# Kernel tuning notes

Measured on AMD Instinct MI355X. Metric: run time of the kernel, lower is better.

The kernel has to match this reference:

```python
import jax, jax.numpy as jnp
import numpy as np

B, S, V, E, H = 128, 128, 8000, 512, 2048
GIVEN = 64


def setup_inputs() -> dict:
    key = jax.random.key(0)
    ks = jax.random.split(key, 13)
    def p(i, shape):
        return (jax.random.normal(ks[i], shape, jnp.float32) * 0.02)
    return {
        "x": jax.random.randint(ks[0], (B, S), 0, V, jnp.int32),
        "class_label": jax.random.randint(ks[1], (B,), 0, 2, jnp.int32),
        "given_num": GIVEN,
        "emb": p(2, (V, E)),
        "Wih0": p(3, (4 * H, E)), "Whh0": p(4, (4 * H, H)),
        "bih0": p(5, (4 * H,)), "bhh0": p(6, (4 * H,)),
        "Wih1": p(7, (4 * H, H)), "Whh1": p(8, (4 * H, H)),
        "bih1": p(9, (4 * H,)), "bhh1": p(10, (4 * H,)),
        "Wlin": p(11, (V, H)), "blin": p(12, (V,)),
    }


def _cell(xt, h, c, Wih, Whh, bih, bhh):
    # PyTorch LSTMCell math, gate order (i, f, g, o)
    g = xt @ Wih.T + h @ Whh.T + (bih + bhh)
    i, f, gg, o = jnp.split(g, 4, axis=-1)
    c = jax.nn.sigmoid(f) * c + jax.nn.sigmoid(i) * jnp.tanh(gg)
    h = jax.nn.sigmoid(o) * jnp.tanh(c)
    return h, c


def reference(x, class_label, given_num, emb, Wih0, Whh0, bih0, bhh0,
              Wih1, Whh1, bih1, bhh1, Wlin, blin):
    Bb, Ss = x.shape
    Hh = Whh0.shape[1]
    z = jnp.zeros((Bb, Hh), dtype=emb.dtype)
    init = (z, z, z, z)  # (h0, c0, h1, c1) for 2-layer LSTM

    def two_layer(carry, te):
        h0, c0, h1, c1 = carry
        h0, c0 = _cell(te, h0, c0, Wih0, Whh0, bih0, bhh0)
        h1, c1 = _cell(h0, h1, c1, Wih1, Whh1, bih1, bhh1)
        return (h0, c0, h1, c1)

    # Teacher-forced prefix: feed ground-truth tokens for i < given_num
    seq_e = emb[x[:, :given_num]]  # (B, given_num, E)
    def tf_step(carry, te):
        return two_layer(carry, te), None
    carry, _ = jax.lax.scan(tf_step, init, seq_e.swapaxes(0, 1))

    # Rollout: sample from softmax(logits) each step (multinomial == categorical)
    te0 = emb[x[:, given_num - 1]]  # (B, E)
    keys = jax.random.split(jax.random.key(1), Ss - given_num)

    def roll_step(carry, k):
        (h0, c0, h1, c1), te = carry
        h0, c0, h1, c1 = two_layer((h0, c0, h1, c1), te)
        logits = h1 @ Wlin.T + blin  # (B, V)
        nt = jax.random.categorical(k, logits)  # (B,)
        return ((h0, c0, h1, c1), emb[nt]), nt

    _, toks = jax.lax.scan(roll_step, (carry, te0), keys)  # (S-given, B)
    return jnp.concatenate([x[:, :given_num], toks.T.astype(x.dtype)], axis=1)
```

## Files before the change

### kernel.cpp

```cpp
#include <hip/hip_runtime.h>
#include <stdint.h>
#include <math.h>

#define B_     128
#define S_     128
#define V_     8000
#define E_     512
#define H_     2048
#define H4_    8192
#define GIVEN_ 64

typedef __bf16 bf16x8 __attribute__((ext_vector_type(8)));
typedef float  f32x16 __attribute__((ext_vector_type(16)));
typedef short  short8 __attribute__((ext_vector_type(8)));

__device__ __forceinline__ uint32_t rotl32(uint32_t v, int d) {
  return (v << d) | (v >> (32 - d));
}

__device__ __forceinline__ void threefry2x32(uint32_t k0, uint32_t k1,
                                             uint32_t x0, uint32_t x1,
                                             uint32_t& o0, uint32_t& o1) {
  uint32_t k2 = k0 ^ k1 ^ 0x1BD11BDAu;
  x0 += k0; x1 += k1;
#define TF_RND(R) { x0 += x1; x1 = rotl32(x1, (R)); x1 ^= x0; }
  TF_RND(13) TF_RND(15) TF_RND(26) TF_RND(6)
  x0 += k1; x1 += k2 + 1u;
  TF_RND(17) TF_RND(29) TF_RND(16) TF_RND(24)
  x0 += k2; x1 += k0 + 2u;
  TF_RND(13) TF_RND(15) TF_RND(26) TF_RND(6)
  x0 += k0; x1 += k1 + 3u;
  TF_RND(17) TF_RND(29) TF_RND(16) TF_RND(24)
  x0 += k1; x1 += k2 + 4u;
  TF_RND(13) TF_RND(15) TF_RND(26) TF_RND(6)
  x0 += k2; x1 += k0 + 5u;
#undef TF_RND
  o0 = x0; o1 = x1;
}

__global__ void keys_kernel(uint32_t* __restrict__ keys) {
  int t = threadIdx.x;
  uint32_t o0, o1;
  threefry2x32(0u, 1u, 0u, (uint32_t)t, o0, o1);
  keys[2 * t]     = o0;
  keys[2 * t + 1] = o1;
}

__global__ void copy_prefix(const int* __restrict__ x, int* __restrict__ out) {
  int idx = blockIdx.x * blockDim.x + threadIdx.x;
  int b = idx >> 6;
  int s = idx & 63;
  out[b * S_ + s] = x[b * S_ + s];
}

__device__ __forceinline__ void split2(float x, uint16_t& hi, uint16_t& lo) {
  uint32_t xb = __float_as_uint(x);
  hi = (uint16_t)(xb >> 16);
  float l = x - __uint_as_float(xb & 0xFFFF0000u);
  lo = (uint16_t)(__float_as_uint(l) >> 16);
}

__device__ __forceinline__ void splitpack(float4 a, float4 b,
                                          bf16x8& hi, bf16x8& lo) {
  float e[8] = {a.x, a.y, a.z, a.w, b.x, b.y, b.z, b.w};
  short8 h, l;
#pragma unroll
  for (int j = 0; j < 8; ++j) {
    uint16_t h16, l16;
    split2(e[j], h16, l16);
    h[j] = (short)h16;
    l[j] = (short)l16;
  }
  hi = __builtin_bit_cast(bf16x8, h);
  lo = __builtin_bit_cast(bf16x8, l);
}

__device__ __forceinline__ void unpack3(short8 hv, uint2 m, bf16x8& bh, bf16x8& bl) {
  short8 lv;
#pragma unroll
  for (int j = 0; j < 8; ++j) {
    uint32_t hbits = ((uint32_t)(uint16_t)hv[j]) << 16;
    uint32_t mbyte = ((j < 4 ? (m.x >> (8 * j)) : (m.y >> (8 * (j - 4)))) & 0xFFu);
    float xf = __uint_as_float(hbits | (mbyte << 8));
    float lf = xf - __uint_as_float(hbits);
    lv[j] = (short)(__float_as_uint(lf) >> 16);
  }
  bh = __builtin_bit_cast(bf16x8, hv);
  bl = __builtin_bit_cast(bf16x8, lv);
}

__global__ void pack3_panel(
    const float* __restrict__ W, uint16_t* __restrict__ PH,
    uint8_t* __restrict__ PM, int K, int nks, int gateRe)
{
  const int bid = blockIdx.x;
  const int jb = bid / nks, ks = bid - jb * nks;
  const int t = threadIdx.x;
  const int lrow = t & 31, lgrp = t >> 5;
  const int wrow = gateRe ? ((lrow >> 3) * H_ + jb * 8 + (lrow & 7))
                          : (jb * 32 + lrow);
  const float* src = W + (size_t)wrow * K + ks * 16 + lgrp * 8;
  float4 a = ((const float4*)src)[0];
  float4 b = ((const float4*)src)[1];
  float e[8] = {a.x, a.y, a.z, a.w, b.x, b.y, b.z, b.w};
  short8 h;
  uint32_t mlo = 0, mhi = 0;
#pragma unroll
  for (int j = 0; j < 8; ++j) {
    uint32_t xb = __float_as_uint(e[j]);
    h[j] = (short)(xb >> 16);
    uint32_t mb = (xb >> 8) & 0xFFu;
    if (j < 4) mlo |= mb << (8 * j);
    else       mhi |= mb << (8 * (j - 4));
  }
  const size_t bi = ((size_t)bid * 64 + t) * 8;
  *(short8*)&PH[bi] = h;
  *(uint2*)&PM[bi] = make_uint2(mlo, mhi);
}

#define MFMA_(a, b, c) __builtin_amdgcn_mfma_f32_32x32x16_bf16(a, b, c, 0, 0, 0)

template<bool GATHER>
__device__ __forceinline__ void run_phase_p(
    f32x16 (&acc)[4],
    const float* __restrict__ aF,
    const uint16_t* __restrict__ aHi, const uint16_t* __restrict__ aLo,
    const int* __restrict__ ridx, int rstride,
    const uint16_t* __restrict__ PH, const uint8_t* __restrict__ PM,
    int K, int jb, int w, int lane, int lrow, int lgrp)
{
  const int nFS = K >> 7;
  const size_t bbase = (size_t)jb * (K >> 4);

  size_t aoff0, aoff1, aoff2, aoff3;
  if (GATHER) {
    aoff0 = (size_t)ridx[(size_t)(lrow)      * rstride] * E_ + lgrp * 8;
    aoff1 = (size_t)ridx[(size_t)(32 + lrow) * rstride] * E_ + lgrp * 8;
    aoff2 = (size_t)ridx[(size_t)(64 + lrow) * rstride] * E_ + lgrp * 8;
    aoff3 = (size_t)ridx[(size_t)(96 + lrow) * rstride] * E_ + lgrp * 8;
  } else {
    aoff0 = (size_t)lgrp * 256 + (size_t)lrow * 8;
    aoff1 = aoff0 + 512;
    aoff2 = aoff0 + 1024;
    aoff3 = aoff0 + 1536;
  }

  short8 bH[4]; uint2 bM[4];
  float4 gR0[2][2], gR1[2][2], gR2[2][2], gR3[2][2];
  bf16x8 sh0[2], sh1[2], sh2[2], sh3[2], sl0[2], sl1[2], sl2[2], sl3[2];

#define BLOAD(BUF, KS)                                                       \
  {                                                                          \
    const size_t bi = ((bbase + (size_t)(KS)) * 64 + (size_t)lane) * 8;      \
    bH[BUF] = *(const short8*)(PH + bi);                                     \
    bM[BUF] = *(const uint2*)(PM + bi);                                      \
  }

#define ALOAD(BUF, KS)                                                       \
  {                                                                          \
    if (GATHER) {                                                            \
      const float* a0 = aF + aoff0 + (size_t)(KS) * 16;                      \
      const float* a1 = aF + aoff1 + (size_t)(KS) * 16;                      \
      const float* a2 = aF + aoff2 + (size_t)(KS) * 16;                      \
      const float* a3 = aF + aoff3 + (size_t)(KS) * 16;                      \
      gR0[BUF][0] = ((const float4*)a0)[0]; gR0[BUF][1] = ((const float4*)a0)[1]; \
      gR1[BUF][0] = ((const float4*)a1)[0]; gR1[BUF][1] = ((const float4*)a1)[1]; \
      gR2[BUF][0] = ((const float4*)a2)[0]; gR2[BUF][1] = ((const float4*)a2)[1]; \
      gR3[BUF][0] = ((const float4*)a3)[0]; gR3[BUF][1] = ((const float4*)a3)[1]; \
    } else {                                                                 \
      size_t o0 = aoff0 + (size_t)(KS) * 2048;                               \
      size_t o1 = aoff1 + (size_t)(KS) * 2048;                               \
      size_t o2 = aoff2 + (size_t)(KS) * 2048;                               \
      size_t o3 = aoff3 + (size_t)(KS) * 2048;                               \
      sh0[BUF] = *(const bf16x8*)(aHi + o0); sl0[BUF] = *(const bf16x8*)(aLo + o0); \
      sh1[BUF] = *(const bf16x8*)(aHi + o1); sl1[BUF] = *(const bf16x8*)(aLo + o1); \
      sh2[BUF] = *(const bf16x8*)(aHi + o2); sl2[BUF] = *(const bf16x8*)(aLo + o2); \
      sh3[BUF] = *(const bf16x8*)(aHi + o3); sl3[BUF] = *(const bf16x8*)(aLo + o3); \
    }                                                                        \
  }

#define COMP(BB, AB)                                                         \
  {                                                                          \
    bf16x8 bh, bl;                                                           \
    unpack3(bH[BB], bM[BB], bh, bl);                                         \
    bf16x8 ah, al;                                                           \
    if (GATHER) splitpack(gR0[AB][0], gR0[AB][1], ah, al);                   \
    else { ah = sh0[AB]; al = sl0[AB]; }                                     \
    acc[0] = MFMA_(ah, bh, acc[0]);                                          \
    acc[0] = MFMA_(ah, bl, acc[0]);                                          \
    acc[0] = MFMA_(al, bh, acc[0]);                                          \
    if (GATHER) splitpack(gR1[AB][0], gR1[AB][1], ah, al);                   \
    else { ah = sh1[AB]; al = sl1[AB]; }                                     \
    acc[1] = MFMA_(ah, bh, acc[1]);                                          \
    acc[1] = MFMA_(ah, bl, acc[1]);                                          \
    acc[1] = MFMA_(al, bh, acc[1]);                                          \
    if (GATHER) splitpack(gR2[AB][0], gR2[AB][1], ah, al);                   \
    else { ah = sh2[AB]; al = sl2[AB]; }                                     \
    acc[2] = MFMA_(ah, bh, acc[2]);                                          \
    acc[2] = MFMA_(ah, bl, acc[2]);                                          \
    acc[2] = MFMA_(al, bh, acc[2]);                                          \
    if (GATHER) splitpack(gR3[AB][0], gR3[AB][1], ah, al);                   \
    else { ah = sh3[AB]; al = sl3[AB]; }                                     \
    acc[3] = MFMA_(ah, bh, acc[3]);                                          \
    acc[3] = MFMA_(ah, bl, acc[3]);                                          \
    acc[3] = MFMA_(al, bh, acc[3]);                                          \
  }

  BLOAD(0, w); BLOAD(1, w + 8); BLOAD(2, w + 16); BLOAD(3, w + 24);
  ALOAD(0, w); ALOAD(1, w + 8);
  for (int it = 0; it < nFS; it += 4) {
    const int kb = w + it * 8;
    COMP(0, 0);
    if (it + 4 < nFS) BLOAD(0, kb + 32);
    if (it + 2 < nFS) ALOAD(0, kb + 16);
    COMP(1, 1);
    if (it + 5 < nFS) BLOAD(1, kb + 40);
    if (it + 3 < nFS) ALOAD(1, kb + 24);
    COMP(2, 0);
    if (it + 6 < nFS) BLOAD(2, kb + 48);
    if (it + 4 < nFS) ALOAD(0, kb + 32);
    COMP(3, 1);
    if (it + 7 < nFS) BLOAD(3, kb + 56);
    if (it + 5 < nFS) ALOAD(1, kb + 40);
  }
#undef BLOAD
#undef ALOAD
#undef COMP
}

template<int EPI, int GATHER1>
__global__ __launch_bounds__(512, 2) void gemm_ks_p(
    const float* __restrict__ a1F,
    const uint16_t* __restrict__ a1Hi, const uint16_t* __restrict__ a1Lo,
    const int* __restrict__ ridx, int rstride,
    const uint16_t* __restrict__ PH1, const uint8_t* __restrict__ PM1, int K1,
    const uint16_t* __restrict__ a2Hi, const uint16_t* __restrict__ a2Lo,
    const uint16_t* __restrict__ PH2, const uint8_t* __restrict__ PM2, int K2,
    const float* __restrict__ bih, const float* __restrict__ bhh,
    float* __restrict__ cState,
    uint16_t* __restrict__ hOutHi, uint16_t* __restrict__ hOutLo,
    const float* __restrict__ bias, float* __restrict__ Cout)
{
  __shared__ float red[4][128 * 32];

  const int jb   = blockIdx.x;
  const int tid  = threadIdx.x;
  const int w    = tid >> 6;
  const int lane = tid & 63;
  const int lrow = lane & 31;
  const int lgrp = lane >> 5;

  f32x16 acc[4];
#pragma unroll
  for (int mf = 0; mf < 4; ++mf)
#pragma unroll
    for (int r = 0; r < 16; ++r) acc[mf][r] = 0.0f;

  run_phase_p<GATHER1 != 0>(acc, a1F, a1Hi, a1Lo, ridx, rstride,
                            PH1, PM1, K1, jb, w, lane, lrow, lgrp);
  if (K2 > 0)
    run_phase_p<false>(acc, nullptr, a2Hi, a2Lo, nullptr, 0,
                       PH2, PM2, K2, jb, w, lane, lrow, lgrp);

  const int wl = w & 3;
  if (w < 4) {
#pragma unroll
    for (int mf = 0; mf < 4; ++mf)
#pragma unroll
      for (int r = 0; r < 16; ++r) {
        const int row = mf * 32 + (r & 3) + 8 * (r >> 2) + 4 * lgrp;
        red[wl][row * 32 + (lrow ^ (row & 31))] = acc[mf][r];
      }
  }
  __syncthreads();
  if (w >= 4) {
#pragma unroll
    for (int mf = 0; mf < 4; ++mf)
#pragma unroll
      for (int r = 0; r < 16; ++r) {
        const int row = mf * 32 + (r & 3) + 8 * (r >> 2) + 4 * lgrp;
        red[wl][row * 32 + (lrow ^ (row & 31))] += acc[mf][r];
      }
  }
  __syncthreads();

  if constexpr (EPI == 1) {
    const int b  = tid & 127;
    const int uh = (tid >> 7) * 2;
#pragma unroll
    for (int q = 0; q < 2; ++q) {
      const int u = uh + q;
      float gs[4];
#pragma unroll
      for (int g = 0; g < 4; ++g) {
        const int cs = (g * 8 + u) ^ (b & 31);
        gs[g] = ((red[0][b * 32 + cs] + red[1][b * 32 + cs])
                 + red[2][b * 32 + cs]) + red[3][b * 32 + cs];
      }
      const int n = jb * 8 + u;
      float gi = gs[0] + bih[n]          + bhh[n];
      float gf = gs[1] + bih[H_ + n]     + bhh[H_ + n];
      float gg = gs[2] + bih[2 * H_ + n] + bhh[2 * H_ + n];
      float go = gs[3] + bih[3 * H_ + n] + bhh[3 * H_ + n];
      float si = 1.f / (1.f + expf(-gi));
      float sf = 1.f / (1.f + expf(-gf));
      float so = 1.f / (1.f + expf(-go));
      const size_t ci = (size_t)b * H_ + n;
      float cv = sf * cState[ci] + si * tanhf(gg);
      cState[ci] = cv;
      float hv = so * tanhf(cv);
      uint16_t hh, hl;
      split2(hv, hh, hl);
      const size_t hoff = (size_t)((n >> 4) * 4 + (b >> 5)) * 512
                        + (size_t)((n >> 3) & 1) * 256
                        + (size_t)(b & 31) * 8 + (size_t)(n & 7);
      hOutHi[hoff] = hh;
      hOutLo[hoff] = hl;
    }
  } else {
    const int b  = tid & 127;
    const int ch = (tid >> 7) * 8;
#pragma unroll
    for (int q = 0; q < 8; ++q) {
      const int col = ch + q;
      const int cs  = col ^ (b & 31);
      float v = ((red[0][b * 32 + cs] + red[1][b * 32 + cs])
                 + red[2][b * 32 + cs]) + red[3][b * 32 + cs];
      Cout[(size_t)b * V_ + jb * 32 + col] = v + bias[jb * 32 + col];
    }
  }
}

__global__ __launch_bounds__(256) void sample_kernel(
    const float* __restrict__ logits, const uint32_t* __restrict__ keys,
    int t, int* __restrict__ out, int col)
{
  const int b = blockIdx.x;
  const int tid = threadIdx.x;
  const uint32_t k0 = keys[2 * t];
  const uint32_t k1 = keys[2 * t + 1];
  const float* lrow = logits + (size_t)b * V_;

  float best = -3.4e38f;
  int bestIdx = 0;
  for (int v = tid; v < V_; v += 256) {
    uint32_t j = (uint32_t)(b * V_ + v);
    uint32_t o0, o1;
    threefry2x32(k0, k1, 0u, j, o0, o1);
    uint32_t bits = o0 ^ o1;
    float f = __uint_as_float((bits >> 9) | 0x3f800000u) - 1.0f;
    float u = fmaxf(1.17549435e-38f, f + 1.17549435e-38f);
    float t1 = (float)log((double)u);
    float t2 = -t1;
    float t3 = (float)log((double)t2);
    float val = (-t3) + lrow[v];
    if (val > best) { best = val; bestIdx = v; }
  }

  __shared__ float sv[256];
  __shared__ int   si[256];
  sv[tid] = best; si[tid] = bestIdx;
  __syncthreads();
  for (int s = 128; s > 0; s >>= 1) {
    if (tid < s) {
      float v2 = sv[tid + s]; int i2 = si[tid + s];
      if (v2 > sv[tid] || (v2 == sv[tid] && i2 < si[tid])) { sv[tid] = v2; si[tid] = i2; }
    }
    __syncthreads();
  }
  if (tid == 0) out[b * S_ + col] = si[0];
}

extern "C" void kernel_launch(void* const* d_in, const int* in_sizes, int n_in,
                              void* d_out, int out_size, void* d_ws, size_t ws_size,
                              hipStream_t stream) {
  const int*   x    = (const int*)  d_in[0];
  const float* emb  = (const float*)d_in[3];
  const float* Wih0 = (const float*)d_in[4];
  const float* Whh0 = (const float*)d_in[5];
  const float* bih0 = (const float*)d_in[6];
  const float* bhh0 = (const float*)d_in[7];
  const float* Wih1 = (const float*)d_in[8];
  const float* Whh1 = (const float*)d_in[9];
  const float* bih1 = (const float*)d_in[10];
  const float* bhh1 = (const float*)d_in[11];
  const float* Wlin = (const float*)d_in[12];
  const float* blin = (const float*)d_in[13];
  int* out = (int*)d_out;

  char* wp = (char*)d_ws;
  size_t o = 0;
  auto alloc = [&](size_t bytes) {
    void* p = wp + o; o += (bytes + 255) & ~(size_t)255; return p;
  };
  uint32_t* keys   = (uint32_t*)alloc(512);
  float*    logits = (float*)   alloc((size_t)B_ * V_ * 4);
  float*    c0     = (float*)   alloc((size_t)B_ * H_ * 4);
  float*    c1     = (float*)   alloc((size_t)B_ * H_ * 4);
  uint16_t* hS0hi[2]; uint16_t* hS0lo[2]; uint16_t* hS1hi[2]; uint16_t* hS1lo[2];
  for (int i = 0; i < 2; ++i) hS0hi[i] = (uint16_t*)alloc((size_t)B_ * H_ * 2);
  for (int i = 0; i < 2; ++i) hS0lo[i] = (uint16_t*)alloc((size_t)B_ * H_ * 2);
  for (int i = 0; i < 2; ++i) hS1hi[i] = (uint16_t*)alloc((size_t)B_ * H_ * 2);
  for (int i = 0; i < 2; ++i) hS1lo[i] = (uint16_t*)alloc((size_t)B_ * H_ * 2);
  size_t zeroBytes = (size_t)((char*)hS1lo[1] + (size_t)B_ * H_ * 2 - (char*)c0);

  const size_t nIh0 = (size_t)H4_ * E_;
  const size_t nHh  = (size_t)H4_ * H_;
  const size_t nLin = (size_t)V_ * H_;
  uint16_t* PHih0 = (uint16_t*)alloc(nIh0 * 2);
  uint8_t*  PMih0 = (uint8_t*) alloc(nIh0);
  uint16_t* PHhh0 = (uint16_t*)alloc(nHh * 2);
  uint8_t*  PMhh0 = (uint8_t*) alloc(nHh);
  uint16_t* PHih1 = (uint16_t*)alloc(nHh * 2);
  uint8_t*  PMih1 = (uint8_t*) alloc(nHh);
  uint16_t* PHhh1 = (uint16_t*)alloc(nHh * 2);
  uint8_t*  PMhh1 = (uint8_t*) alloc(nHh);
  uint16_t* PHlin = (uint16_t*)alloc(nLin * 2);
  uint8_t*  PMlin = (uint8_t*) alloc(nLin);

  hipMemsetAsync(c0, 0, zeroBytes, stream);
  keys_kernel<<<1, 64, 0, stream>>>(keys);
  copy_prefix<<<(B_ * GIVEN_) / 256, 256, 0, stream>>>(x, out);
  pack3_panel<<<256 * 32,  64, 0, stream>>>(Wih0, PHih0, PMih0, E_, 32, 1);
  pack3_panel<<<256 * 128, 64, 0, stream>>>(Whh0, PHhh0, PMhh0, H_, 128, 1);
  pack3_panel<<<256 * 128, 64, 0, stream>>>(Wih1, PHih1, PMih1, H_, 128, 1);
  pack3_panel<<<256 * 128, 64, 0, stream>>>(Whh1, PHhh1, PMhh1, H_, 128, 1);
  pack3_panel<<<250 * 128, 64, 0, stream>>>(Wlin, PHlin, PMlin, H_, 128, 0);

  int p = 0;
  auto lstm_step = [&](const int* ridx) {
    gemm_ks_p<1, 1><<<H_ / 8, 512, 0, stream>>>(
        emb, nullptr, nullptr, ridx, S_, PHih0, PMih0, E_,
        hS0hi[p], hS0lo[p], PHhh0, PMhh0, H_,
        bih0, bhh0, c0, hS0hi[p ^ 1], hS0lo[p ^ 1], nullptr, nullptr);
    gemm_ks_p<1, 0><<<H_ / 8, 512, 0, stream>>>(
        nullptr, hS0hi[p ^ 1], hS0lo[p ^ 1], nullptr, 0, PHih1, PMih1, H_,
        hS1hi[p], hS1lo[p], PHhh1, PMhh1, H_,
        bih1, bhh1, c1, hS1hi[p ^ 1], hS1lo[p ^ 1], nullptr, nullptr);
    p ^= 1;
  };

  for (int t = 0; t < GIVEN_; ++t) {
    lstm_step(x + t);
  }

  for (int t = 0; t < S_ - GIVEN_; ++t) {
    const int* ridx = (t == 0) ? (x + (GIVEN_ - 1)) : (out + (GIVEN_ + t - 1));
    lstm_step(ridx);
    gemm_ks_p<0, 0><<<V_ / 32, 512, 0, stream>>>(
        nullptr, hS1hi[p], hS1lo[p], nullptr, 0, PHlin, PMlin, H_,
        nullptr, nullptr, nullptr, nullptr, 0,
        nullptr, nullptr, nullptr, nullptr, nullptr, blin, logits);
    sample_kernel<<<B_, 256, 0, stream>>>(logits, keys, t, out, GIVEN_ + t);
  }
}
```

Baseline: 11.30 ms.

## Split K across 16 waves per block with 1024-thread GEMM launches

Doubles the threads per block from 512 to 1024, so each GEMM block splits its K reduction across 16 waves instead of 8 and each wave handles half as many K slices. The deeper 4-stage B prefetch ring is replaced by a simpler 2-stage double buffer that loads A and B together. The cross-wave reduction now runs in four synchronised rounds through shared memory, and each epilogue thread handles one output column instead of two (or four instead of eight). The goal is more waves in flight per block to hide memory latency on these small-batch GEMMs. The cost is more __syncthreads rounds, less prefetch depth, and only one block per CU under the new launch bounds.

```diff
diff --git a/kernel.cpp b/kernel.cpp
--- a/kernel.cpp
+++ b/kernel.cpp
@@ -129,7 +129,7 @@
     const uint16_t* __restrict__ PH, const uint8_t* __restrict__ PM,
     int K, int jb, int w, int lane, int lrow, int lgrp)
 {
-  const int nFS = K >> 7;
+  const int nFS = K >> 8;
   const size_t bbase = (size_t)jb * (K >> 4);
 
   size_t aoff0, aoff1, aoff2, aoff3;
@@ -145,19 +145,15 @@
     aoff3 = aoff0 + 1536;
   }
 
-  short8 bH[4]; uint2 bM[4];
+  short8 bH[2]; uint2 bM[2];
   float4 gR0[2][2], gR1[2][2], gR2[2][2], gR3[2][2];
   bf16x8 sh0[2], sh1[2], sh2[2], sh3[2], sl0[2], sl1[2], sl2[2], sl3[2];
 
-#define BLOAD(BUF, KS)                                                       \
+#define LOADFS(BUF, KS)                                                      \
   {                                                                          \
     const size_t bi = ((bbase + (size_t)(KS)) * 64 + (size_t)lane) * 8;      \
     bH[BUF] = *(const short8*)(PH + bi);                                     \
     bM[BUF] = *(const uint2*)(PM + bi);                                      \
-  }
-
-#define ALOAD(BUF, KS)                                                       \
-  {                                                                          \
     if (GATHER) {                                                            \
       const float* a0 = aF + aoff0 + (size_t)(KS) * 16;                      \
       const float* a1 = aF + aoff1 + (size_t)(KS) * 16;                      \
@@ -179,57 +175,49 @@
     }                                                                        \
   }
 
-#define COMP(BB, AB)                                                         \
+#define COMPFS(BUF)                                                          \
   {                                                                          \
     bf16x8 bh, bl;                                                           \
-    unpack3(bH[BB], bM[BB], bh, bl);                                         \
+    unpack3(bH[BUF], bM[BUF], bh, bl);                                       \
     bf16x8 ah, al;                                                           \
-    if (GATHER) splitpack(gR0[AB][0], gR0[AB][1], ah, al);                   \
-    else { ah = sh0[AB]; al = sl0[AB]; }                                     \
+    if (GATHER) splitpack(gR0[BUF][0], gR0[BUF][1], ah, al);                 \
+    else { ah = sh0[BUF]; al = sl0[BUF]; }                                   \
     acc[0] = MFMA_(ah, bh, acc[0]);                                          \
     acc[0] = MFMA_(ah, bl, acc[0]);                                          \
     acc[0] = MFMA_(al, bh, acc[0]);                                          \
-    if (GATHER) splitpack(gR1[AB][0], gR1[AB][1], ah, al);                   \
-    else { ah = sh1[AB]; al = sl1[AB]; }                                     \
+    if (GATHER) splitpack(gR1[BUF][0], gR1[BUF][1], ah, al);                 \
+    else { ah = sh1[BUF]; al = sl1[BUF]; }                                   \
     acc[1] = MFMA_(ah, bh, acc[1]);                                          \
     acc[1] = MFMA_(ah, bl, acc[1]);                                          \
     acc[1] = MFMA_(al, bh, acc[1]);                                          \
-    if (GATHER) splitpack(gR2[AB][0], gR2[AB][1], ah, al);                   \
-    else { ah = sh2[AB]; al = sl2[AB]; }                                     \
+    if (GATHER) splitpack(gR2[BUF][0], gR2[BUF][1], ah, al);                 \
+    else { ah = sh2[BUF]; al = sl2[BUF]; }                                   \
     acc[2] = MFMA_(ah, bh, acc[2]);                                          \
     acc[2] = MFMA_(ah, bl, acc[2]);                                          \
     acc[2] = MFMA_(al, bh, acc[2]);                                          \
-    if (GATHER) splitpack(gR3[AB][0], gR3[AB][1], ah, al);                   \
-    else { ah = sh3[AB]; al = sl3[AB]; }                                     \
+    if (GATHER) splitpack(gR3[BUF][0], gR3[BUF][1], ah, al);                 \
+    else { ah = sh3[BUF]; al = sl3[BUF]; }                                   \
     acc[3] = MFMA_(ah, bh, acc[3]);                                          \
     acc[3] = MFMA_(ah, bl, acc[3]);                                          \
     acc[3] = MFMA_(al, bh, acc[3]);                                          \
   }
 
-  BLOAD(0, w); BLOAD(1, w + 8); BLOAD(2, w + 16); BLOAD(3, w + 24);
-  ALOAD(0, w); ALOAD(1, w + 8);
-  for (int it = 0; it < nFS; it += 4) {
-    const int kb = w + it * 8;
-    COMP(0, 0);
-    if (it + 4 < nFS) BLOAD(0, kb + 32);
-    if (it + 2 < nFS) ALOAD(0, kb + 16);
-    COMP(1, 1);
-    if (it + 5 < nFS) BLOAD(1, kb + 40);
-    if (it + 3 < nFS) ALOAD(1, kb + 24);
-    COMP(2, 0);
-    if (it + 6 < nFS) BLOAD(2, kb + 48);
-    if (it + 4 < nFS) ALOAD(0, kb + 32);
-    COMP(3, 1);
-    if (it + 7 < nFS) BLOAD(3, kb + 56);
-    if (it + 5 < nFS) ALOAD(1, kb + 40);
-  }
-#undef BLOAD
-#undef ALOAD
-#undef COMP
+  int ks = w;
+  LOADFS(0, ks); ks += 16;
+  int rem = nFS;
+  while (rem >= 2) {
+    LOADFS(1, ks); ks += 16;
+    COMPFS(0);
+    if (rem > 2) { LOADFS(0, ks); ks += 16; }
+    COMPFS(1);
+    rem -= 2;
+  }
+#undef LOADFS
+#undef COMPFS
 }
 
 template<int EPI, int GATHER1>
-__global__ __launch_bounds__(512, 2) void gemm_ks_p(
+__global__ __launch_bounds__(1024, 1) void gemm_ks_p(
     const float* __restrict__ a1F,
     const uint16_t* __restrict__ a1Hi, const uint16_t* __restrict__ a1Lo,
     const int* __restrict__ ridx, int rstride,
@@ -263,65 +251,56 @@
                        PH2, PM2, K2, jb, w, lane, lrow, lgrp);
 
   const int wl = w & 3;
-  if (w < 4) {
-#pragma unroll
-    for (int mf = 0; mf < 4; ++mf)
-#pragma unroll
-      for (int r = 0; r < 16; ++r) {
-        const int row = mf * 32 + (r & 3) + 8 * (r >> 2) + 4 * lgrp;
-        red[wl][row * 32 + (lrow ^ (row & 31))] = acc[mf][r];
-      }
-  }
-  __syncthreads();
-  if (w >= 4) {
-#pragma unroll
-    for (int mf = 0; mf < 4; ++mf)
-#pragma unroll
-      for (int r = 0; r < 16; ++r) {
-        const int row = mf * 32 + (r & 3) + 8 * (r >> 2) + 4 * lgrp;
-        red[wl][row * 32 + (lrow ^ (row & 31))] += acc[mf][r];
-      }
-  }
-  __syncthreads();
+  const int wg = w >> 2;
+#pragma unroll
+  for (int g = 0; g < 4; ++g) {
+    if (wg == g) {
+#pragma unroll
+      for (int mf = 0; mf < 4; ++mf)
+#pragma unroll
+        for (int r = 0; r < 16; ++r) {
+          const int row = mf * 32 + (r & 3) + 8 * (r >> 2) + 4 * lgrp;
+          if (g == 0) red[wl][row * 32 + (lrow ^ (row & 31))]  = acc[mf][r];
+          else        red[wl][row * 32 + (lrow ^ (row & 31))] += acc[mf][r];
+        }
+    }
+    __syncthreads();
+  }
 
   if constexpr (EPI == 1) {
-    const int b  = tid & 127;
-    const int uh = (tid >> 7) * 2;
-#pragma unroll
-    for (int q = 0; q < 2; ++q) {
-      const int u = uh + q;
-      float gs[4];
-#pragma unroll
-      for (int g = 0; g < 4; ++g) {
-        const int cs = (g * 8 + u) ^ (b & 31);
-        gs[g] = ((red[0][b * 32 + cs] + red[1][b * 32 + cs])
-                 + red[2][b * 32 + cs]) + red[3][b * 32 + cs];
-      }
-      const int n = jb * 8 + u;
-      float gi = gs[0] + bih[n]          + bhh[n];
-      float gf = gs[1] + bih[H_ + n]     + bhh[H_ + n];
-      float gg = gs[2] + bih[2 * H_ + n] + bhh[2 * H_ + n];
-      float go = gs[3] + bih[3 * H_ + n] + bhh[3 * H_ + n];
-      float si = 1.f / (1.f + expf(-gi));
-      float sf = 1.f / (1.f + expf(-gf));
-      float so = 1.f / (1.f + expf(-go));
-      const size_t ci = (size_t)b * H_ + n;
-      float cv = sf * cState[ci] + si * tanhf(gg);
-      cState[ci] = cv;
-      float hv = so * tanhf(cv);
-      uint16_t hh, hl;
-      split2(hv, hh, hl);
-      const size_t hoff = (size_t)((n >> 4) * 4 + (b >> 5)) * 512
-                        + (size_t)((n >> 3) & 1) * 256
-                        + (size_t)(b & 31) * 8 + (size_t)(n & 7);
-      hOutHi[hoff] = hh;
-      hOutLo[hoff] = hl;
+    const int b = tid & 127;
+    const int u = tid >> 7;
+    float gs[4];
+#pragma unroll
+    for (int g = 0; g < 4; ++g) {
+      const int cs = (g * 8 + u) ^ (b & 31);
+      gs[g] = ((red[0][b * 32 + cs] + red[1][b * 32 + cs])
+               + red[2][b * 32 + cs]) + red[3][b * 32 + cs];
     }
+    const int n = jb * 8 + u;
+    float gi = gs[0] + bih[n]          + bhh[n];
+    float gf = gs[1] + bih[H_ + n]     + bhh[H_ + n];
+    float gg = gs[2] + bih[2 * H_ + n] + bhh[2 * H_ + n];
+    float go = gs[3] + bih[3 * H_ + n] + bhh[3 * H_ + n];
+    float si = 1.f / (1.f + expf(-gi));
+    float sf = 1.f / (1.f + expf(-gf));
+    float so = 1.f / (1.f + expf(-go));
+    const size_t ci = (size_t)b * H_ + n;
+    float cv = sf * cState[ci] + si * tanhf(gg);
+    cState[ci] = cv;
+    float hv = so * tanhf(cv);
+    uint16_t hh, hl;
+    split2(hv, hh, hl);
+    const size_t hoff = (size_t)((n >> 4) * 4 + (b >> 5)) * 512
+                      + (size_t)((n >> 3) & 1) * 256
+                      + (size_t)(b & 31) * 8 + (size_t)(n & 7);
+    hOutHi[hoff] = hh;
+    hOutLo[hoff] = hl;
   } else {
     const int b  = tid & 127;
-    const int ch = (tid >> 7) * 8;
-#pragma unroll
-    for (int q = 0; q < 8; ++q) {
+    const int ch = (tid >> 7) * 4;
+#pragma unroll
+    for (int q = 0; q < 4; ++q) {
       const int col = ch + q;
       const int cs  = col ^ (b & 31);
       float v = ((red[0][b * 32 + cs] + red[1][b * 32 + cs])
@@ -429,11 +408,11 @@
 
   int p = 0;
   auto lstm_step = [&](const int* ridx) {
-    gemm_ks_p<1, 1><<<H_ / 8, 512, 0, stream>>>(
+    gemm_ks_p<1, 1><<<H_ / 8, 1024, 0, stream>>>(
         emb, nullptr, nullptr, ridx, S_, PHih0, PMih0, E_,
         hS0hi[p], hS0lo[p], PHhh0, PMhh0, H_,
         bih0, bhh0, c0, hS0hi[p ^ 1], hS0lo[p ^ 1], nullptr, nullptr);
-    gemm_ks_p<1, 0><<<H_ / 8, 512, 0, stream>>>(
+    gemm_ks_p<1, 0><<<H_ / 8, 1024, 0, stream>>>(
         nullptr, hS0hi[p ^ 1], hS0lo[p ^ 1], nullptr, 0, PHih1, PMih1, H_,
         hS1hi[p], hS1lo[p], PHhh1, PMhh1, H_,
         bih1, bhh1, c1, hS1hi[p ^ 1], hS1lo[p ^ 1], nullptr, nullptr);
@@ -447,7 +426,7 @@
   for (int t = 0; t < S_ - GIVEN_; ++t) {
     const int* ridx = (t == 0) ? (x + (GIVEN_ - 1)) : (out + (GIVEN_ + t - 1));
     lstm_step(ridx);
-    gemm_ks_p<0, 0><<<V_ / 32, 512, 0, stream>>>(
+    gemm_ks_p<0, 0><<<V_ / 32, 1024, 0, stream>>>(
         nullptr, hS1hi[p], hS1lo[p], nullptr, 0, PHlin, PMlin, H_,
         nullptr, nullptr, nullptr, nullptr, 0,
         nullptr, nullptr, nullptr, nullptr, nullptr, blin, logits);
```

New measurement: 34.76 ms. 208% more time.
